# Kernel tuning notes

Hardware: AMD Instinct MI355X
Metric: run time of the kernel (lower is better)

The kernel has to match this reference:

```python
import jax, jax.numpy as jnp
import numpy as np

DIM = 256
HEADS = 8
DIM_HEAD = 32
INNER = HEADS * DIM_HEAD  # 256
EPS = 1e-5


def layer_norm(x, g, b):
    mu = jnp.mean(x, axis=-1, keepdims=True)
    var = jnp.var(x, axis=-1, keepdims=True)
    return (x - mu) * jax.lax.rsqrt(var + EPS) * g + b


def setup_inputs() -> dict:
    key = jax.random.key(0)
    ks = jax.random.split(key, 8)
    b, l, gx, gy, w1, w2 = 2, 5, 6, 8, 8, 8
    B, N = b * gx * gy, l * w1 * w2  # 96, 320
    x = jax.random.normal(ks[0], (b, l, gx, gy, w1, w2, DIM), dtype=jnp.float32)
    # context is the additive attention bias: [B, N, heads*N] -> (B,h,N,N)
    context = jax.random.normal(ks[1], (B, N, HEADS * N), dtype=jnp.float32) * 0.1
    s = 1.0 / np.sqrt(DIM)
    w_q = jax.random.normal(ks[2], (DIM, INNER), dtype=jnp.float32) * s
    w_kv = jax.random.normal(ks[3], (DIM, 2 * INNER), dtype=jnp.float32) * s
    w_out = jax.random.normal(ks[4], (INNER, DIM_HEAD), dtype=jnp.float32) * (1.0 / np.sqrt(INNER))
    ln_g = jnp.ones((DIM,), dtype=jnp.float32)
    ln_b = jnp.zeros((DIM,), dtype=jnp.float32)
    return {"x": x, "context": context, "w_q": w_q, "w_kv": w_kv,
            "w_out": w_out, "ln_g": ln_g, "ln_b": ln_b}


def reference(x, context, w_q, w_kv, w_out, ln_g, ln_b):
    b, l, gx, gy, w1, w2, d = x.shape
    # 'b l x y w1 w2 d -> (b x y) (l w1 w2) d'
    xs = jnp.transpose(x, (0, 2, 3, 1, 4, 5, 6)).reshape(b * gx * gy, l * w1 * w2, d)
    B, N, D = xs.shape
    xs = layer_norm(xs, ln_g, ln_b)
    q = (xs @ w_q).reshape(B, N, HEADS, DIM_HEAD).transpose(0, 2, 1, 3)   # b h n d
    kv = xs @ w_kv
    k, v = jnp.split(kv, 2, axis=-1)
    k = k.reshape(B, N, HEADS, DIM_HEAD).transpose(0, 2, 1, 3)
    v = v.reshape(B, N, HEADS, DIM_HEAD).transpose(0, 2, 1, 3)
    # bias mode with context: dots = q k^T (unscaled, faithful to source) + bias
    dots = jnp.einsum('bhnd,bhmd->bhnm', q, k)
    bias = context.reshape(B, N, HEADS, N).transpose(0, 2, 1, 3)          # b h n m
    dots = dots + bias
    attn = jax.nn.softmax(dots, axis=-1)
    out = jnp.einsum('bhnm,bhmd->bhnd', attn, v)                          # b h n d
    # 'b h (l w1 w2) d -> b l w1 w2 (h d)'
    out = out.transpose(0, 2, 1, 3).reshape(B, l, w1, w2, INNER)
    out = out @ w_out                                                     # -> dim_head
    # '(b x y) l w1 w2 d -> b l x y w1 w2 d'
    out = out.reshape(b, gx, gy, l, w1, w2, DIM_HEAD).transpose(0, 3, 1, 2, 4, 5, 6)
    return out
```

## Files before the change

kernel.cpp:

```cpp
#include <hip/hip_runtime.h>
#include <hip/hip_bf16.h>

#define BWIN 96
#define NTOK 320
#define DIMX 256
#define HEADS 8
#define DH 32
#define INNER 256
#define CTXW 2560
#define MPAD 328
#define ROWS_T 30720

typedef __bf16 bf16x8 __attribute__((ext_vector_type(8)));
typedef __bf16 bf16x4 __attribute__((ext_vector_type(4)));
typedef float f32x4 __attribute__((ext_vector_type(4)));

__global__ __launch_bounds__(256) void k_pre(
    const float* __restrict__ wq, const float* __restrict__ wkv,
    const float* __restrict__ x, const float* __restrict__ g,
    const float* __restrict__ bt, __bf16* __restrict__ wT,
    __bf16* __restrict__ y)
{
    const int t = threadIdx.x;
    if (blockIdx.x < 768) {
        const int col = blockIdx.x;
        float v;
        if (col < 256)      v = wq[t * 256 + col];
        else if (col < 512) v = wkv[t * 512 + (col - 256)];
        else                v = wkv[t * 512 + 256 + (col - 512)];
        wT[(size_t)col * 256 + t] = (__bf16)v;
        return;
    }
    const int wave = t >> 6, lane = t & 63;
    const int row = (blockIdx.x - 768) * 4 + wave;
    const int bb = row / NTOK, n = row % NTOK;
    const int b_idx = bb / 48, x_idx = (bb % 48) >> 3, y_idx = bb & 7;
    const int l_idx = n >> 6, w1_idx = (n >> 3) & 7, w2_idx = n & 7;
    const size_t src =
        ((((((size_t)b_idx * 5 + l_idx) * 6 + x_idx) * 8 + y_idx) * 8 + w1_idx) * 8 + w2_idx) * (size_t)DIMX;

    const float4 xv = *(const float4*)(x + src + lane * 4);
    float s = xv.x + xv.y + xv.z + xv.w;
    float ss = xv.x * xv.x + xv.y * xv.y + xv.z * xv.z + xv.w * xv.w;
    #pragma unroll
    for (int o = 32; o > 0; o >>= 1) {
        s += __shfl_xor(s, o);
        ss += __shfl_xor(ss, o);
    }
    const float mu = s * (1.0f / DIMX);
    const float var = ss * (1.0f / DIMX) - mu * mu;
    const float rsig = rsqrtf(var + 1e-5f);
    const float4 g4 = *(const float4*)(g + lane * 4);
    const float4 b4 = *(const float4*)(bt + lane * 4);
    bf16x4 yo;
    yo[0] = (__bf16)((xv.x - mu) * rsig * g4.x + b4.x);
    yo[1] = (__bf16)((xv.y - mu) * rsig * g4.y + b4.y);
    yo[2] = (__bf16)((xv.z - mu) * rsig * g4.z + b4.z);
    yo[3] = (__bf16)((xv.w - mu) * rsig * g4.w + b4.w);
    *(bf16x4*)(y + (size_t)row * DIMX + lane * 4) = yo;
}

__global__ __launch_bounds__(256) void k_qkv(
    const __bf16* __restrict__ y, const __bf16* __restrict__ wT,
    __bf16* __restrict__ qhb, __bf16* __restrict__ khb, __bf16* __restrict__ vhb)
{
    __shared__ __bf16 yls[128][40];
    __shared__ __bf16 wls[128][40];
    const int t = threadIdx.x, wave = t >> 6, lane = t & 63;
    const int lr = lane & 15, lg = lane >> 4;
    const int wm = wave & 1, wn = wave >> 1;
    const int rbase = blockIdx.x * 128;
    const int cbase = blockIdx.y * 128;

    f32x4 acc[4][4];
    #pragma unroll
    for (int im = 0; im < 4; ++im)
        #pragma unroll
        for (int jn = 0; jn < 4; ++jn) acc[im][jn] = (f32x4){0.f, 0.f, 0.f, 0.f};

    const int srow = t >> 1, sseg = (t & 1) * 16;
    #pragma unroll
    for (int ks = 0; ks < 8; ++ks) {
        __syncthreads();
        #pragma unroll
        for (int j = 0; j < 2; ++j) {
            *(bf16x8*)&yls[srow][sseg + j * 8] =
                *(const bf16x8*)(y + (size_t)(rbase + srow) * DIMX + ks * 32 + sseg + j * 8);
            *(bf16x8*)&wls[srow][sseg + j * 8] =
                *(const bf16x8*)(wT + (size_t)(cbase + srow) * DIMX + ks * 32 + sseg + j * 8);
        }
        __syncthreads();

        bf16x8 yfr[4], wfr[4];
        #pragma unroll
        for (int jn = 0; jn < 4; ++jn) yfr[jn] = *(const bf16x8*)&yls[wm * 64 + jn * 16 + lr][lg * 8];
        #pragma unroll
        for (int im = 0; im < 4; ++im) wfr[im] = *(const bf16x8*)&wls[wn * 64 + im * 16 + lr][lg * 8];
        #pragma unroll
        for (int im = 0; im < 4; ++im)
            #pragma unroll
            for (int jn = 0; jn < 4; ++jn)
                acc[im][jn] = __builtin_amdgcn_mfma_f32_16x16x32_bf16(wfr[im], yfr[jn], acc[im][jn], 0, 0, 0);
    }

    #pragma unroll
    for (int im = 0; im < 4; ++im) {
        const int g = cbase + wn * 64 + im * 16 + lg * 4;
        const int which = g >> 8;
        __bf16* buf = (which == 0) ? qhb : (which == 1) ? khb : vhb;
        const int hh = (g & 255) >> 5, d = g & 31;
        #pragma unroll
        for (int jn = 0; jn < 4; ++jn) {
            const int row = rbase + wm * 64 + jn * 16 + lr;
            const int bb2 = row / NTOK, n2 = row % NTOK;
            bf16x4 p;
            #pragma unroll
            for (int i = 0; i < 4; ++i) p[i] = (__bf16)acc[im][jn][i];
            *(bf16x4*)(buf + ((size_t)(bb2 * 8 + hh) * NTOK + n2) * DH + d) = p;
        }
    }
}

__global__ __launch_bounds__(128) void k_attn(
    const __bf16* __restrict__ qhb, const __bf16* __restrict__ khb,
    const __bf16* __restrict__ vhb, const float* __restrict__ wout,
    const float* __restrict__ ctx, float* __restrict__ part)
{
    __shared__ __bf16 vwls[DH][MPAD];
    __shared__ __bf16 ctxls[2][16][MPAD];
    const int t = threadIdx.x, wave = t >> 6, lane = t & 63;
    const int lr = lane & 15, lg = lane >> 4;
    const int h = blockIdx.x & 7, bb = blockIdx.x >> 3;
    const size_t panel = (size_t)(bb * 8 + h);

    {
        bf16x8 afr[2];
        #pragma unroll
        for (int rt = 0; rt < 2; ++rt)
            #pragma unroll
            for (int j = 0; j < 8; ++j)
                afr[rt][j] = (__bf16)wout[(h * 32 + lg * 8 + j) * 32 + rt * 16 + lr];
        const __bf16* vbase = vhb + panel * NTOK * DH + lg * 8;
        #pragma unroll
        for (int mt = 0; mt < 10; ++mt) {
            const int m = wave * 160 + mt * 16 + lr;
            const bf16x8 bfr = *(const bf16x8*)(vbase + (size_t)m * DH);
            #pragma unroll
            for (int rt = 0; rt < 2; ++rt) {
                const f32x4 d4 = __builtin_amdgcn_mfma_f32_16x16x32_bf16(
                    afr[rt], bfr, (f32x4){0.f, 0.f, 0.f, 0.f}, 0, 0, 0);
                #pragma unroll
                for (int i = 0; i < 4; ++i)
                    vwls[rt * 16 + lg * 4 + i][wave * 160 + mt * 16 + lr] = (__bf16)d4[i];
            }
        }
    }
    __syncthreads();

    const float* cpan = ctx + (size_t)bb * NTOK * CTXW + h * NTOK;
    const __bf16* qpan = qhb + panel * NTOK * DH;
    const __bf16* kpan = khb + panel * NTOK * DH;
    float* ppan = part + ((size_t)h * ROWS_T + (size_t)bb * NTOK) * DH;

    float4 creg[20];
    {
        const float* cb = cpan + (size_t)(wave * 16) * CTXW;
        #pragma unroll
        for (int j = 0; j < 20; ++j) {
            const int f = j * 64 + lane, r = f / 80, c = f % 80;
            creg[j] = *(const float4*)(cb + (size_t)r * CTXW + c * 4);
        }
    }

    for (int it = 0; it < 10; ++it) {
        const int nw = (it * 2 + wave) * 16;

        #pragma unroll
        for (int j = 0; j < 20; ++j) {
            const int f = j * 64 + lane, r = f / 80, c = f % 80;
            bf16x4 b;
            b[0] = (__bf16)creg[j].x; b[1] = (__bf16)creg[j].y;
            b[2] = (__bf16)creg[j].z; b[3] = (__bf16)creg[j].w;
            *(bf16x4*)&ctxls[wave][r][c * 4] = b;
        }
        if (it < 9) {
            const float* cb = cpan + (size_t)((it * 2 + 2 + wave) * 16) * CTXW;
            #pragma unroll
            for (int j = 0; j < 20; ++j) {
                const int f = j * 64 + lane, r = f / 80, c = f % 80;
                creg[j] = *(const float4*)(cb + (size_t)r * CTXW + c * 4);
            }
        }

        const bf16x8 qfrag = *(const bf16x8*)(qpan + (size_t)(nw + lr) * DH + lg * 8);

        f32x4 s[20];
        #pragma unroll
        for (int mt = 0; mt < 20; ++mt) {
            const bf16x8 kfrag = *(const bf16x8*)(kpan + (size_t)(mt * 16 + lr) * DH + lg * 8);
            s[mt] = __builtin_amdgcn_mfma_f32_16x16x32_bf16(kfrag, qfrag,
                                                            (f32x4){0.f, 0.f, 0.f, 0.f}, 0, 0, 0);
        }

        #pragma unroll
        for (int mt = 0; mt < 20; ++mt) {
            const bf16x4 c4 = *(const bf16x4*)&ctxls[wave][lr][mt * 16 + lg * 4];
            #pragma unroll
            for (int i = 0; i < 4; ++i) s[mt][i] += (float)c4[i];
        }

        float mx = -3e38f;
        #pragma unroll
        for (int mt = 0; mt < 20; ++mt)
            #pragma unroll
            for (int i = 0; i < 4; ++i) mx = fmaxf(mx, s[mt][i]);
        mx = fmaxf(mx, __shfl_xor(mx, 16));
        mx = fmaxf(mx, __shfl_xor(mx, 32));

        float sum = 0.f;
        #pragma unroll
        for (int mt = 0; mt < 20; ++mt) {
            bf16x4 p4;
            #pragma unroll
            for (int i = 0; i < 4; ++i) {
                const float e = __expf(s[mt][i] - mx);
                sum += e;
                p4[i] = (__bf16)e;
            }
            *(bf16x4*)&ctxls[wave][lr][mt * 16 + lg * 4] = p4;
        }
        sum += __shfl_xor(sum, 16);
        sum += __shfl_xor(sum, 32);
        const float rinv = 1.0f / sum;

        f32x4 o0 = {0.f, 0.f, 0.f, 0.f}, o1 = {0.f, 0.f, 0.f, 0.f};
        #pragma unroll
        for (int ks = 0; ks < 10; ++ks) {
            const bf16x8 pfrag = *(const bf16x8*)&ctxls[wave][lr][ks * 32 + lg * 8];
            const bf16x8 vf0 = *(const bf16x8*)&vwls[lr][ks * 32 + lg * 8];
            const bf16x8 vf1 = *(const bf16x8*)&vwls[16 + lr][ks * 32 + lg * 8];
            o0 = __builtin_amdgcn_mfma_f32_16x16x32_bf16(vf0, pfrag, o0, 0, 0, 0);
            o1 = __builtin_amdgcn_mfma_f32_16x16x32_bf16(vf1, pfrag, o1, 0, 0, 0);
        }

        float* pdst = ppan + (size_t)(nw + lr) * DH + lg * 4;
        f32x4 r0, r1;
        #pragma unroll
        for (int i = 0; i < 4; ++i) { r0[i] = o0[i] * rinv; r1[i] = o1[i] * rinv; }
        *(f32x4*)(pdst)      = r0;
        *(f32x4*)(pdst + 16) = r1;
    }
}

__global__ __launch_bounds__(256) void k_red(
    const float* __restrict__ part, float* __restrict__ out)
{
    const int idx = blockIdx.x * 256 + threadIdx.x;
    const int row = idx >> 3, q4 = (idx & 7) * 4;
    f32x4 a = {0.f, 0.f, 0.f, 0.f};
    #pragma unroll
    for (int h = 0; h < HEADS; ++h) {
        const f32x4 p = *(const f32x4*)(part + ((size_t)h * ROWS_T + row) * DH + q4);
        #pragma unroll
        for (int i = 0; i < 4; ++i) a[i] += p[i];
    }
    const int bb = row / NTOK, n = row % NTOK;
    const int b_idx = bb / 48, x_idx = (bb % 48) >> 3, y_idx = bb & 7;
    const int l_idx = n >> 6, w1_idx = (n >> 3) & 7, w2_idx = n & 7;
    const size_t dst =
        ((((((size_t)b_idx * 5 + l_idx) * 6 + x_idx) * 8 + y_idx) * 8 + w1_idx) * 8 + w2_idx) * (size_t)DH;
    *(f32x4*)(out + dst + q4) = a;
}

extern "C" void kernel_launch(void* const* d_in, const int* in_sizes, int n_in,
                              void* d_out, int out_size, void* d_ws, size_t ws_size,
                              hipStream_t stream) {
    const float* x    = (const float*)d_in[0];
    const float* ctx  = (const float*)d_in[1];
    const float* wq   = (const float*)d_in[2];
    const float* wkv  = (const float*)d_in[3];
    const float* wout = (const float*)d_in[4];
    const float* ln_g = (const float*)d_in[5];
    const float* ln_b = (const float*)d_in[6];
    float* out = (float*)d_out;

    const size_t SEG = (size_t)BWIN * NTOK * INNER;
    __bf16* qhb = (__bf16*)d_ws;
    __bf16* khb = qhb + SEG;
    __bf16* vhb = khb + SEG;
    __bf16* yb  = vhb + SEG;
    __bf16* wT  = yb + SEG;
    float*  part = (float*)(wT + 768 * 256);

    const int ROWS = BWIN * NTOK;
    k_pre<<<768 + ROWS / 4, 256, 0, stream>>>(wq, wkv, x, ln_g, ln_b, wT, yb);
    k_qkv<<<dim3(ROWS / 128, 6), 256, 0, stream>>>(yb, wT, qhb, khb, vhb);
    k_attn<<<BWIN * HEADS, 128, 0, stream>>>(qhb, khb, vhb, wout, ctx, part);
    k_red<<<ROWS * 8 / 256, 256, 0, stream>>>(part, out);
}
```

Measured before the change: 154.6 us.

## Fuse head reduction into attention via atomics and swizzle QKV block order

Removes the separate reduction kernel and the per-head partial buffer: each attention block now atomically adds its head's projected output straight into the final permuted output, which is zeroed with a memset first. The QKV GEMM grid is flattened to one dimension and remapped so blocks are spread across XCDs by row/column tile. This trades a partial-buffer write/read plus a kernel launch for 8-way float atomic contention per output element and an extra memset. Float atomics also make the summation order nondeterministic.

```diff
diff --git a/kernel.cpp b/kernel.cpp
--- a/kernel.cpp
+++ b/kernel.cpp
@@ -69,8 +69,10 @@
     const int t = threadIdx.x, wave = t >> 6, lane = t & 63;
     const int lr = lane & 15, lg = lane >> 4;
     const int wm = wave & 1, wn = wave >> 1;
-    const int rbase = blockIdx.x * 128;
-    const int cbase = blockIdx.y * 128;
+    const int bid = blockIdx.x;
+    const int l2 = (bid & 7) * 180 + (bid >> 3);
+    const int rbase = (l2 / 6) * 128;
+    const int cbase = (l2 % 6) * 128;
 
     f32x4 acc[4][4];
     #pragma unroll
@@ -124,7 +126,7 @@
 __global__ __launch_bounds__(128) void k_attn(
     const __bf16* __restrict__ qhb, const __bf16* __restrict__ khb,
     const __bf16* __restrict__ vhb, const float* __restrict__ wout,
-    const float* __restrict__ ctx, float* __restrict__ part)
+    const float* __restrict__ ctx, float* __restrict__ out)
 {
     __shared__ __bf16 vwls[DH][MPAD];
     __shared__ __bf16 ctxls[2][16][MPAD];
@@ -160,7 +162,8 @@
     const float* cpan = ctx + (size_t)bb * NTOK * CTXW + h * NTOK;
     const __bf16* qpan = qhb + panel * NTOK * DH;
     const __bf16* kpan = khb + panel * NTOK * DH;
-    float* ppan = part + ((size_t)h * ROWS_T + (size_t)bb * NTOK) * DH;
+
+    const int b_idx = bb / 48, x_idx = (bb % 48) >> 3, y_idx = bb & 7;
 
     float4 creg[20];
     {
@@ -243,33 +246,19 @@
             o1 = __builtin_amdgcn_mfma_f32_16x16x32_bf16(vf1, pfrag, o1, 0, 0, 0);
         }
 
-        float* pdst = ppan + (size_t)(nw + lr) * DH + lg * 4;
-        f32x4 r0, r1;
-        #pragma unroll
-        for (int i = 0; i < 4; ++i) { r0[i] = o0[i] * rinv; r1[i] = o1[i] * rinv; }
-        *(f32x4*)(pdst)      = r0;
-        *(f32x4*)(pdst + 16) = r1;
-    }
-}
-
-__global__ __launch_bounds__(256) void k_red(
-    const float* __restrict__ part, float* __restrict__ out)
-{
-    const int idx = blockIdx.x * 256 + threadIdx.x;
-    const int row = idx >> 3, q4 = (idx & 7) * 4;
-    f32x4 a = {0.f, 0.f, 0.f, 0.f};
-    #pragma unroll
-    for (int h = 0; h < HEADS; ++h) {
-        const f32x4 p = *(const f32x4*)(part + ((size_t)h * ROWS_T + row) * DH + q4);
-        #pragma unroll
-        for (int i = 0; i < 4; ++i) a[i] += p[i];
-    }
-    const int bb = row / NTOK, n = row % NTOK;
-    const int b_idx = bb / 48, x_idx = (bb % 48) >> 3, y_idx = bb & 7;
-    const int l_idx = n >> 6, w1_idx = (n >> 3) & 7, w2_idx = n & 7;
-    const size_t dst =
-        ((((((size_t)b_idx * 5 + l_idx) * 6 + x_idx) * 8 + y_idx) * 8 + w1_idx) * 8 + w2_idx) * (size_t)DH;
-    *(f32x4*)(out + dst + q4) = a;
+        const int n = nw + lr;
+        const int l_idx = n >> 6, w1_idx = (n >> 3) & 7, w2_idx = n & 7;
+        const size_t dst =
+            ((((((size_t)b_idx * 5 + l_idx) * 6 + x_idx) * 8 + y_idx) * 8 + w1_idx) * 8 + w2_idx) * (size_t)DH;
+        float* oA = out + dst + lg * 4;
+        #pragma unroll
+        for (int i = 0; i < 4; ++i) {
+            __hip_atomic_fetch_add(oA + i,      o0[i] * rinv,
+                                   __ATOMIC_RELAXED, __HIP_MEMORY_SCOPE_AGENT);
+            __hip_atomic_fetch_add(oA + 16 + i, o1[i] * rinv,
+                                   __ATOMIC_RELAXED, __HIP_MEMORY_SCOPE_AGENT);
+        }
+    }
 }
 
 extern "C" void kernel_launch(void* const* d_in, const int* in_sizes, int n_in,
@@ -290,11 +279,12 @@
     __bf16* vhb = khb + SEG;
     __bf16* yb  = vhb + SEG;
     __bf16* wT  = yb + SEG;
-    float*  part = (float*)(wT + 768 * 256);
 
     const int ROWS = BWIN * NTOK;
+
+    hipMemsetAsync(out, 0, (size_t)out_size * sizeof(float), stream);
+
     k_pre<<<768 + ROWS / 4, 256, 0, stream>>>(wq, wkv, x, ln_g, ln_b, wT, yb);
-    k_qkv<<<dim3(ROWS / 128, 6), 256, 0, stream>>>(yb, wT, qhb, khb, vhb);
-    k_attn<<<BWIN * HEADS, 128, 0, stream>>>(qhb, khb, vhb, wout, ctx, part);
-    k_red<<<ROWS * 8 / 256, 256, 0, stream>>>(part, out);
-}
+    k_qkv<<<1440, 256, 0, stream>>>(yb, wT, qhb, khb, vhb);
+    k_attn<<<BWIN * HEADS, 128, 0, stream>>>(qhb, khb, vhb, wout, ctx, out);
+}
```

Result: slower. 201.1 us (+30.1%).
